# Kernel tuning notes

Measured on AMD Instinct MI355X. Metric: run time of the kernel, lower is better.

Reference implementation:

```python
import jax, jax.numpy as jnp
import numpy as np


def setup_inputs() -> dict:
    key = jax.random.key(0)
    k1, k2 = jax.random.split(key)
    b, n, d = 4, 4096, 512
    m = 4096
    l = max(n, m)
    x = jax.random.normal(k1, (b, n, d), dtype=jnp.float32)
    t = jax.random.normal(k2, (1, 2 * l - 2, d), dtype=jnp.float32)
    return {"x": x, "t": t, "m": m}


def reference(x, t, m):
    # x: (b, n, d); t: (1, 2*max(n,m)-2, d); output: (b, m, d)
    n = x.shape[1]
    l = max(n, m)
    fft_len = 2 * l
    x_fft = jnp.fft.rfft(x, fft_len, axis=-2)   # (b, l+1, d) complex
    t_fft = jnp.fft.rfft(t, fft_len, axis=-2)   # (1, l+1, d) complex
    o = jnp.fft.irfft(x_fft * t_fft, fft_len, axis=-2)[:, :m]
    return o
```

## Files before the change

### kernel.cpp

```cpp
#include <hip/hip_runtime.h>
#include <math.h>

#define N_FFT   8192
#define SEQ     4096
#define NCH     512
#define TLEN    8190

__device__ __forceinline__ float2 cmul(float2 a, float2 b) {
    return make_float2(a.x * b.x - a.y * b.y, a.x * b.y + a.y * b.x);
}
__device__ __forceinline__ float2 cmulj(float2 a, float2 b) {
    return make_float2(a.x * b.x + a.y * b.y, a.y * b.x - a.x * b.y);
}
__device__ __forceinline__ float2 cadd(float2 a, float2 b) {
    return make_float2(a.x + b.x, a.y + b.y);
}
__device__ __forceinline__ float2 csub(float2 a, float2 b) {
    return make_float2(a.x - b.x, a.y - b.y);
}

constexpr float W32C[16] = {
    1.0f, 0.9807852804032304f, 0.9238795325112867f, 0.8314696123025452f,
    0.7071067811865476f, 0.5555702330196023f, 0.3826834323650898f, 0.1950903220161283f,
    0.0f, -0.1950903220161282f, -0.3826834323650897f, -0.5555702330196020f,
    -0.7071067811865475f, -0.8314696123025453f, -0.9238795325112867f, -0.9807852804032304f
};
constexpr float W32S[16] = {
    -0.0f, -0.1950903220161283f, -0.3826834323650898f, -0.5555702330196022f,
    -0.7071067811865476f, -0.8314696123025452f, -0.9238795325112867f, -0.9807852804032304f,
    -1.0f, -0.9807852804032304f, -0.9238795325112867f, -0.8314696123025453f,
    -0.7071067811865476f, -0.5555702330196022f, -0.3826834323650899f, -0.1950903220161286f
};

constexpr int BREV5[32] = {0,16,8,24,4,20,12,28,2,18,10,26,6,22,14,30,
                           1,17,9,25,5,21,13,29,3,19,11,27,7,23,15,31};
constexpr int BREV4[16] = {0,8,4,12,2,10,6,14,1,9,5,13,3,11,7,15};

__device__ __forceinline__ int brev3i(int b) {
    return ((b & 1) << 2) | (b & 2) | ((b & 4) >> 2);
}

__device__ __forceinline__ void fft32_dif(float2 a[32]) {
#pragma unroll
    for (int s = 4; s >= 0; --s) {
        const int h = 1 << s;
#pragma unroll
        for (int g = 0; g < 32; g += 2 * h) {
#pragma unroll
            for (int i = 0; i < h; ++i) {
                float2 x0 = a[g + i], x1 = a[g + i + h];
                a[g + i] = cadd(x0, x1);
                float2 w = make_float2(W32C[i << (4 - s)], W32S[i << (4 - s)]);
                a[g + i + h] = cmul(csub(x0, x1), w);
            }
        }
    }
}

__device__ __forceinline__ void fft16_dif(float2 a[16]) {
#pragma unroll
    for (int s = 3; s >= 0; --s) {
        const int h = 1 << s;
#pragma unroll
        for (int g = 0; g < 16; g += 2 * h) {
#pragma unroll
            for (int i = 0; i < h; ++i) {
                float2 x0 = a[g + i], x1 = a[g + i + h];
                a[g + i] = cadd(x0, x1);
                float2 w = make_float2(W32C[i << (4 - s)], W32S[i << (4 - s)]);
                a[g + i + h] = cmul(csub(x0, x1), w);
            }
        }
    }
}

__device__ __forceinline__ void ifft16_dit(float2 a[16]) {
#pragma unroll
    for (int s = 0; s <= 3; ++s) {
        const int h = 1 << s;
#pragma unroll
        for (int g = 0; g < 16; g += 2 * h) {
#pragma unroll
            for (int i = 0; i < h; ++i) {
                float2 w = make_float2(W32C[i << (4 - s)], -W32S[i << (4 - s)]);
                float2 t = cmul(a[g + i + h], w);
                float2 x0 = a[g + i];
                a[g + i] = cadd(x0, t);
                a[g + i + h] = csub(x0, t);
            }
        }
    }
}

__device__ __forceinline__ void fft8_dif(float2 a[8]) {
#pragma unroll
    for (int s = 2; s >= 0; --s) {
        const int h = 1 << s;
#pragma unroll
        for (int g = 0; g < 8; g += 2 * h) {
#pragma unroll
            for (int i = 0; i < h; ++i) {
                float2 x0 = a[g + i], x1 = a[g + i + h];
                a[g + i] = cadd(x0, x1);
                int e = (i << (2 - s)) << 2;
                float2 w = make_float2(W32C[e], W32S[e]);
                a[g + i + h] = cmul(csub(x0, x1), w);
            }
        }
    }
}

__device__ __forceinline__ int SLOT(int r, int c) {
    return (r << 8) + (c ^ ((c >> 4) & 7) ^ ((r & 1) << 3));
}
__device__ __forceinline__ int ZADDR(int q) {
    return SLOT(q & 31, (((q >> 5) & 31) << 3) + brev3i((q >> 10) & 7));
}
__device__ __forceinline__ int SLOT16(int r, int c) {
    return (r << 8) + (c ^ ((c >> 4) & 7) ^ ((r & 1) << 3));
}

__global__ __launch_bounds__(256) void twiddle_init(float2* __restrict__ tw) {
    int k = blockIdx.x * 256 + threadIdx.x;
    double th = -2.0 * 3.14159265358979323846 * (double)k / (double)N_FFT;
    tw[k] = make_float2((float)cos(th), (float)sin(th));
}

__global__ __launch_bounds__(256) void transpose_in(const float* __restrict__ x,
                                                    const float* __restrict__ t,
                                                    float2* __restrict__ xT,
                                                    float2* __restrict__ tT) {
    __shared__ float tX[64][65], tY[64][65];
    const int tid = threadIdx.x;
    if (blockIdx.x < 1024) {
        const int bid = blockIdx.x;
        const int pb = bid >> 9;
        const int dt = (bid >> 6) & 7;
        const int nt = bid & 63;
        const int d0 = dt << 6, n0 = nt << 6;
        const float* x0 = x + (size_t)(2 * pb) * SEQ * NCH;
        const float* x1 = x0 + (size_t)SEQ * NCH;
        {
            const int c4 = tid & 15, r16 = tid >> 4;
#pragma unroll
            for (int it = 0; it < 4; ++it) {
                int row = r16 + (it << 4);
                size_t off = (size_t)(n0 + row) * NCH + d0 + (c4 << 2);
                float4 v0 = *(const float4*)(x0 + off);
                float4 v1 = *(const float4*)(x1 + off);
                tX[row][(c4 << 2) + 0] = v0.x; tX[row][(c4 << 2) + 1] = v0.y;
                tX[row][(c4 << 2) + 2] = v0.z; tX[row][(c4 << 2) + 3] = v0.w;
                tY[row][(c4 << 2) + 0] = v1.x; tY[row][(c4 << 2) + 1] = v1.y;
                tY[row][(c4 << 2) + 2] = v1.z; tY[row][(c4 << 2) + 3] = v1.w;
            }
        }
        __syncthreads();
        {
            const int nc = tid & 63, dr4 = tid >> 6;
#pragma unroll
            for (int it = 0; it < 16; ++it) {
                int dr = dr4 + (it << 2);
                xT[(((size_t)(pb * NCH + d0 + dr)) << 12) + n0 + nc] =
                    make_float2(tX[nc][dr], tY[nc][dr]);
            }
        }
    } else {
        const int bid = blockIdx.x - 1024;
        const int nt = bid >> 2, dpt = bid & 3;
        const int n0 = nt << 6, dp0 = dpt << 6;
        {
            const int c = tid & 63, r4 = tid >> 6;
#pragma unroll
            for (int it = 0; it < 16; ++it) {
                int row = r4 + (it << 2);
                int nn = n0 + row;
                float2 v = make_float2(0.f, 0.f);
                if (nn < TLEN)
                    v = *(const float2*)(t + (size_t)nn * NCH + ((dp0 + c) << 1));
                tX[row][c] = v.x;
                tY[row][c] = v.y;
            }
        }
        __syncthreads();
        {
            const int nc = tid & 63, dr4 = tid >> 6;
#pragma unroll
            for (int it = 0; it < 16; ++it) {
                int dr = dr4 + (it << 2);
                tT[(((size_t)(dp0 + dr)) << 13) + n0 + nc] =
                    make_float2(tX[nc][dr], tY[nc][dr]);
            }
        }
    }
}

__global__ __launch_bounds__(256) void tfft3_kernel(const float2* __restrict__ tT,
                                                    const float2* __restrict__ tw,
                                                    float2* __restrict__ Tc) {
    __shared__ float2 z[N_FFT];
    const int tid = threadIdx.x;
    const int d0 = blockIdx.x * 2;
    const int d1 = d0 + 1;
    const float2* tp = tT + ((size_t)blockIdx.x << 13);

    float2 a[32];
#pragma unroll
    for (int n1 = 0; n1 < 32; ++n1)
        a[n1] = tp[(n1 << 8) + tid];
    fft32_dif(a);
    {
        float2 w = tw[tid], w2 = cmul(w, w);
        float2 we = make_float2(1.f, 0.f), wo = w;
#pragma unroll
        for (int k1 = 0; k1 < 32; k1 += 2) {
            z[SLOT(k1, tid)]     = (k1 == 0) ? a[0] : cmul(a[BREV5[k1]], we);
            z[SLOT(k1 + 1, tid)] = cmul(a[BREV5[k1 + 1]], wo);
            we = cmul(we, w2); wo = cmul(wo, w2);
        }
    }
    __syncthreads();

    {
        const int r = tid >> 3, n2p = tid & 7;
#pragma unroll
        for (int n1p = 0; n1p < 32; ++n1p)
            a[n1p] = z[SLOT(r, (n1p << 3) + n2p)];
        fft32_dif(a);
        float2 wb = tw[n2p << 5], wb2 = cmul(wb, wb);
        float2 be = make_float2(1.f, 0.f), bo = wb;
#pragma unroll
        for (int k1p = 0; k1p < 32; k1p += 2) {
            z[SLOT(r, (k1p << 3) + n2p)]       = (k1p == 0) ? a[0] : cmul(a[BREV5[k1p]], be);
            z[SLOT(r, ((k1p + 1) << 3) + n2p)] = cmul(a[BREV5[k1p + 1]], bo);
            be = cmul(be, wb2); bo = cmul(bo, wb2);
        }
    }
    __syncthreads();

#pragma unroll
    for (int u = 0; u < 4; ++u) {
        int f = tid + (u << 8);
        int k1 = f >> 5, k1p = f & 31;
        float2 b[8];
#pragma unroll
        for (int e = 0; e < 8; ++e) b[e] = z[SLOT(k1, (k1p << 3) + e)];
        fft8_dif(b);
#pragma unroll
        for (int j = 0; j < 8; ++j) z[SLOT(k1, (k1p << 3) + j)] = b[j];
    }
    __syncthreads();

    const float sc = 0.5f / (float)N_FFT;
#pragma unroll
    for (int v = 0; v < 16; ++v) {
        int p = tid + (v << 8);
        int q   = p >> 9;
        int rem = p & 511;
        int t_  = rem >> 1, e = rem & 1;
        int j_  = (q << 1) + e;
        int kp  = (t_ >> 4) + ((t_ & 15) << 4) + (BREV4[j_] << 8);
#pragma unroll
        for (int par = 0; par < 2; ++par) {
            int k  = 2 * kp + par;
            int km = (N_FFT - k) & (N_FFT - 1);
            float2 A = z[ZADDR(k)];
            float2 B = z[ZADDR(km)];
            float2 Bj = make_float2(B.x, -B.y);
            float2 T0 = make_float2((A.x + Bj.x) * sc, (A.y + Bj.y) * sc);
            float2 dd = csub(A, Bj);
            float2 T1 = make_float2(dd.y * sc, -dd.x * sc);
            Tc[(size_t)d0 * N_FFT + (par << 12) + p] = T0;
            Tc[(size_t)d1 * N_FFT + (par << 12) + p] = T1;
        }
    }
}

__global__ __launch_bounds__(512, 2) void conv5_kernel(float2* __restrict__ xoT,
                                                       const float2* __restrict__ tw,
                                                       const float2* __restrict__ Tc) {
    __shared__ float2 z[2 * SEQ];
    const int tid = threadIdx.x;
    const int par = tid >> 8;
    const int t   = tid & 255;
    const int d   = blockIdx.x;
    float2* zb = z + (par << 12);

    float2 a[16];

#pragma unroll
    for (int pb = 0; pb < 2; ++pb) {
        if (pb == 1) __syncthreads();
        const float2* xp = xoT + ((size_t)(pb * NCH + d) << 12);

        if (par == 0) {
#pragma unroll
            for (int n1 = 0; n1 < 16; ++n1)
                a[n1] = xp[(n1 << 8) + t];
        } else {
#pragma unroll
            for (int n1 = 0; n1 < 16; ++n1)
                a[n1] = cmul(xp[(n1 << 8) + t], tw[(n1 << 8) + t]);
        }
        fft16_dif(a);
        {
            float2 w = tw[2 * t];
            float2 w2 = cmul(w, w);
            float2 we = make_float2(1.f, 0.f), wo = w;
#pragma unroll
            for (int k1 = 0; k1 < 16; k1 += 2) {
                zb[SLOT16(k1, t)]     = (k1 == 0) ? a[0] : cmul(a[BREV4[k1]], we);
                zb[SLOT16(k1 + 1, t)] = cmul(a[BREV4[k1 + 1]], wo);
                we = cmul(we, w2); wo = cmul(wo, w2);
            }
        }
        __syncthreads();

        {
            const int k1 = t >> 4, n3 = t & 15;
#pragma unroll
            for (int n2 = 0; n2 < 16; ++n2)
                a[n2] = zb[SLOT16(k1, (n2 << 4) + n3)];
            fft16_dif(a);
            float2 wb = tw[n3 << 5];
            float2 wb2 = cmul(wb, wb);
            float2 be = make_float2(1.f, 0.f), bo = wb;
#pragma unroll
            for (int r1 = 0; r1 < 16; r1 += 2) {
                zb[SLOT16(k1, (r1 << 4) + n3)]       = (r1 == 0) ? a[0] : cmul(a[BREV4[r1]], be);
                zb[SLOT16(k1, ((r1 + 1) << 4) + n3)] = cmul(a[BREV4[r1 + 1]], bo);
                be = cmul(be, wb2); bo = cmul(bo, wb2);
            }
        }
        __builtin_amdgcn_sched_barrier(0);

        {
            const int k1 = t >> 4, r1 = t & 15;
#pragma unroll
            for (int n3 = 0; n3 < 16; ++n3)
                a[n3] = zb[SLOT16(k1, (r1 << 4) + n3)];
            fft16_dif(a);
            const float4* tp = (const float4*)(Tc + ((size_t)d << 13) + (par << 12));
#pragma unroll
            for (int q = 0; q < 8; ++q) {
                float4 f4 = tp[(q << 8) + t];
                a[2 * q]     = cmul(a[2 * q],     make_float2(f4.x, f4.y));
                a[2 * q + 1] = cmul(a[2 * q + 1], make_float2(f4.z, f4.w));
            }
            ifft16_dit(a);
#pragma unroll
            for (int n3 = 0; n3 < 16; ++n3)
                zb[SLOT16(k1, (r1 << 4) + n3)] = a[n3];
        }
        __builtin_amdgcn_sched_barrier(0);

        {
            const int k1 = t >> 4, n3 = t & 15;
            float2 wb = tw[n3 << 5], wb2 = cmul(wb, wb);
            float2 be = make_float2(1.f, 0.f), bo = wb;
#pragma unroll
            for (int r1 = 0; r1 < 16; r1 += 2) {
                float2 v0 = zb[SLOT16(k1, (r1 << 4) + n3)];
                float2 v1 = zb[SLOT16(k1, ((r1 + 1) << 4) + n3)];
                a[BREV4[r1]]     = (r1 == 0) ? v0 : cmulj(v0, be);
                a[BREV4[r1 + 1]] = cmulj(v1, bo);
                be = cmul(be, wb2); bo = cmul(bo, wb2);
            }
            ifft16_dit(a);
#pragma unroll
            for (int n2 = 0; n2 < 16; ++n2)
                zb[SLOT16(k1, (n2 << 4) + n3)] = a[n2];
        }
        __syncthreads();

        {
            float2 w = tw[2 * t], w2 = cmul(w, w);
            float2 we = make_float2(1.f, 0.f), wo = w;
#pragma unroll
            for (int k1 = 0; k1 < 16; k1 += 2) {
                float2 v0 = zb[SLOT16(k1, t)];
                float2 v1 = zb[SLOT16(k1 + 1, t)];
                a[BREV4[k1]]     = (k1 == 0) ? v0 : cmulj(v0, we);
                a[BREV4[k1 + 1]] = cmulj(v1, wo);
                we = cmul(we, w2); wo = cmul(wo, w2);
            }
            ifft16_dit(a);
        }
        __syncthreads();

        if (par == 0) {
#pragma unroll
            for (int n1 = 8; n1 < 16; ++n1)
                zb[((n1 - 8) << 8) + t] = a[n1];
        } else {
#pragma unroll
            for (int n1 = 0; n1 < 8; ++n1)
                zb[(n1 << 8) + t] = a[n1];
        }
        __syncthreads();

        {
            float2* xw = xoT + ((size_t)(pb * NCH + d) << 12);
            if (par == 0) {
#pragma unroll
                for (int n1 = 0; n1 < 8; ++n1) {
                    int n = (n1 << 8) + t;
                    float2 uo = z[SEQ + (n1 << 8) + t];
                    xw[n] = cadd(a[n1], cmulj(uo, tw[n]));
                }
            } else {
#pragma unroll
                for (int n1 = 8; n1 < 16; ++n1) {
                    int n = (n1 << 8) + t;
                    float2 ue = z[((n1 - 8) << 8) + t];
                    xw[n] = cadd(ue, cmulj(a[n1], tw[n]));
                }
            }
        }
    }
}

__global__ __launch_bounds__(256) void transpose_out(const float2* __restrict__ oT,
                                                     float* __restrict__ out) {
    __shared__ float2 tile[32][65];
    const int tid = threadIdx.x;
    const int bid = blockIdx.x;
    const int pb = bid >> 10;
    const int dt = (bid >> 6) & 15;
    const int nt = bid & 63;
    const int d0 = dt << 5, n0 = nt << 6;

    {
        const int nl = tid & 63, dl = tid >> 6;
#pragma unroll
        for (int i = 0; i < 8; ++i) {
            int dd = dl + (i << 2);
            tile[dd][nl] = oT[(((size_t)(pb * NCH + d0 + dd)) << 12) + n0 + nl];
        }
    }
    __syncthreads();
    {
        const int dl = tid & 31, ns = tid >> 5;
        float* o0 = out + (size_t)(2 * pb) * SEQ * NCH;
        float* o1 = o0 + (size_t)SEQ * NCH;
#pragma unroll
        for (int j = 0; j < 8; ++j) {
            int nn = n0 + ns + (j << 3);
            float2 v = tile[dl][ns + (j << 3)];
            o0[(size_t)nn * NCH + d0 + dl] = v.x;
            o1[(size_t)nn * NCH + d0 + dl] = v.y;
        }
    }
}

__global__ __launch_bounds__(256) void tfft2_kernel(const float* __restrict__ t,
                                                    const float2* __restrict__ tw,
                                                    float2* __restrict__ Tc) {
    __shared__ float2 z[N_FFT];
    const int tid = threadIdx.x;
    const int d0 = blockIdx.x * 2;
    const int d1 = d0 + 1;

    float2 a[32];
#pragma unroll
    for (int n1 = 0; n1 < 32; ++n1) {
        int n = (n1 << 8) + tid;
        float va = 0.f, vb = 0.f;
        if (n < TLEN) {
            va = t[(size_t)n * NCH + d0];
            vb = t[(size_t)n * NCH + d1];
        }
        a[n1] = make_float2(va, vb);
    }
    fft32_dif(a);
    {
        float2 w = tw[tid], w2 = cmul(w, w);
        float2 we = make_float2(1.f, 0.f), wo = w;
#pragma unroll
        for (int k1 = 0; k1 < 32; k1 += 2) {
            z[SLOT(k1, tid)]     = (k1 == 0) ? a[0] : cmul(a[BREV5[k1]], we);
            z[SLOT(k1 + 1, tid)] = cmul(a[BREV5[k1 + 1]], wo);
            we = cmul(we, w2); wo = cmul(wo, w2);
        }
    }
    __syncthreads();
    {
        const int r = tid >> 3, n2p = tid & 7;
#pragma unroll
        for (int n1p = 0; n1p < 32; ++n1p)
            a[n1p] = z[SLOT(r, (n1p << 3) + n2p)];
        fft32_dif(a);
        float2 wb = tw[n2p << 5], wb2 = cmul(wb, wb);
        float2 be = make_float2(1.f, 0.f), bo = wb;
#pragma unroll
        for (int k1p = 0; k1p < 32; k1p += 2) {
            z[SLOT(r, (k1p << 3) + n2p)]       = (k1p == 0) ? a[0] : cmul(a[BREV5[k1p]], be);
            z[SLOT(r, ((k1p + 1) << 3) + n2p)] = cmul(a[BREV5[k1p + 1]], bo);
            be = cmul(be, wb2); bo = cmul(bo, wb2);
        }
    }
    __syncthreads();
#pragma unroll
    for (int u = 0; u < 4; ++u) {
        int f = tid + (u << 8);
        int k1 = f >> 5, k1p = f & 31;
        float2 b[8];
#pragma unroll
        for (int e = 0; e < 8; ++e) b[e] = z[SLOT(k1, (k1p << 3) + e)];
        fft8_dif(b);
#pragma unroll
        for (int j = 0; j < 8; ++j) z[SLOT(k1, (k1p << 3) + j)] = b[j];
    }
    __syncthreads();

    const float sc = 0.5f / (float)N_FFT;
#pragma unroll
    for (int v = 0; v < 16; ++v) {
        int s = tid + (v << 8);
        int k1 = s >> 8, r1 = (s >> 4) & 15, j = s & 15;
        int kp = k1 + (r1 << 4) + (BREV4[j] << 8);
#pragma unroll
        for (int par = 0; par < 2; ++par) {
            int k  = 2 * kp + par;
            int km = (N_FFT - k) & (N_FFT - 1);
            float2 A = z[ZADDR(k)];
            float2 B = z[ZADDR(km)];
            float2 Bj = make_float2(B.x, -B.y);
            float2 T0 = make_float2((A.x + Bj.x) * sc, (A.y + Bj.y) * sc);
            float2 dd = csub(A, Bj);
            float2 T1 = make_float2(dd.y * sc, -dd.x * sc);
            Tc[(size_t)d0 * N_FFT + (par << 12) + s] = T0;
            Tc[(size_t)d1 * N_FFT + (par << 12) + s] = T1;
        }
    }
}

template<bool OT>
__global__ __launch_bounds__(256, 2) void conv3_kernel(const float* __restrict__ x,
                                                       const float2* __restrict__ tw,
                                                       const float2* __restrict__ Tc,
                                                       float2* __restrict__ oT,
                                                       float* __restrict__ out) {
    __shared__ float2 z[SEQ];
    const int tid = threadIdx.x;
    const int sb = (blockIdx.x & 7) * 128 + (blockIdx.x >> 3);
    const int d  = sb >> 1;
    const int pb = sb & 1;

    const float* x0 = x + (size_t)(2 * pb) * SEQ * NCH + d;
    const float* x1 = x0 + (size_t)SEQ * NCH;

    float2 a[16], ie[16];

#pragma unroll
    for (int par = 0; par < 2; ++par) {
        if (par == 1) __syncthreads();

        if (par == 0) {
#pragma unroll
            for (int n1 = 0; n1 < 16; ++n1) {
                int n = (n1 << 8) + tid;
                a[n1] = make_float2(x0[(size_t)n * NCH], x1[(size_t)n * NCH]);
            }
        } else {
#pragma unroll
            for (int n1 = 0; n1 < 16; ++n1) {
                int n = (n1 << 8) + tid;
                float2 v = make_float2(x0[(size_t)n * NCH], x1[(size_t)n * NCH]);
                a[n1] = cmul(v, tw[n]);
            }
        }
        fft16_dif(a);
        {
            float2 w = tw[2 * tid], w2 = cmul(w, w);
            float2 we = make_float2(1.f, 0.f), wo = w;
#pragma unroll
            for (int k1 = 0; k1 < 16; k1 += 2) {
                z[SLOT16(k1, tid)]     = (k1 == 0) ? a[0] : cmul(a[BREV4[k1]], we);
                z[SLOT16(k1 + 1, tid)] = cmul(a[BREV4[k1 + 1]], wo);
                we = cmul(we, w2); wo = cmul(wo, w2);
            }
        }
        __syncthreads();
        {
            const int k1 = tid >> 4, n3 = tid & 15;
#pragma unroll
            for (int n2 = 0; n2 < 16; ++n2)
                a[n2] = z[SLOT16(k1, (n2 << 4) + n3)];
            fft16_dif(a);
            float2 wb = tw[n3 << 5], wb2 = cmul(wb, wb);
            float2 be = make_float2(1.f, 0.f), bo = wb;
#pragma unroll
            for (int r1 = 0; r1 < 16; r1 += 2) {
                z[SLOT16(k1, (r1 << 4) + n3)]       = (r1 == 0) ? a[0] : cmul(a[BREV4[r1]], be);
                z[SLOT16(k1, ((r1 + 1) << 4) + n3)] = cmul(a[BREV4[r1 + 1]], bo);
                be = cmul(be, wb2); bo = cmul(bo, wb2);
            }
        }
        __syncthreads();
        {
            const int k1 = tid >> 4, r1 = tid & 15;
#pragma unroll
            for (int n3 = 0; n3 < 16; ++n3)
                a[n3] = z[SLOT16(k1, (r1 << 4) + n3)];
            fft16_dif(a);
            const float2* Td = Tc + ((size_t)d << 13) + (par << 12);
#pragma unroll
            for (int j = 0; j < 16; ++j) {
                float2 T = Td[(tid << 4) + j];
                a[j] = cmul(a[j], T);
            }
            ifft16_dit(a);
#pragma unroll
            for (int n3 = 0; n3 < 16; ++n3)
                z[SLOT16(k1, (r1 << 4) + n3)] = a[n3];
        }
        __syncthreads();
        {
            const int k1 = tid >> 4, n3 = tid & 15;
            float2 wb = tw[n3 << 5], wb2 = cmul(wb, wb);
            float2 be = make_float2(1.f, 0.f), bo = wb;
#pragma unroll
            for (int r1 = 0; r1 < 16; r1 += 2) {
                float2 v0 = z[SLOT16(k1, (r1 << 4) + n3)];
                float2 v1 = z[SLOT16(k1, ((r1 + 1) << 4) + n3)];
                a[BREV4[r1]]     = (r1 == 0) ? v0 : cmulj(v0, be);
                a[BREV4[r1 + 1]] = cmulj(v1, bo);
                be = cmul(be, wb2); bo = cmul(bo, wb2);
            }
            ifft16_dit(a);
#pragma unroll
            for (int n2 = 0; n2 < 16; ++n2)
                z[SLOT16(k1, (n2 << 4) + n3)] = a[n2];
        }
        __syncthreads();
        {
            float2 w = tw[2 * tid], w2 = cmul(w, w);
            float2 we = make_float2(1.f, 0.f), wo = w;
#pragma unroll
            for (int k1 = 0; k1 < 16; k1 += 2) {
                float2 v0 = z[SLOT16(k1, tid)];
                float2 v1 = z[SLOT16(k1 + 1, tid)];
                a[BREV4[k1]]     = (k1 == 0) ? v0 : cmulj(v0, we);
                a[BREV4[k1 + 1]] = cmulj(v1, wo);
                we = cmul(we, w2); wo = cmul(wo, w2);
            }
            ifft16_dit(a);
        }

        if (par == 0) {
#pragma unroll
            for (int n1 = 0; n1 < 16; ++n1) ie[n1] = a[n1];
        } else {
            if constexpr (OT) {
                float2* op = oT + (((size_t)(pb * NCH + d)) << 12);
#pragma unroll
                for (int n1 = 0; n1 < 16; ++n1) {
                    int n = (n1 << 8) + tid;
                    op[n] = cadd(ie[n1], cmulj(a[n1], tw[n]));
                }
            } else {
                float* o0 = out + (size_t)(2 * pb) * SEQ * NCH + d;
                float* o1 = o0 + (size_t)SEQ * NCH;
#pragma unroll
                for (int n1 = 0; n1 < 16; ++n1) {
                    int n = (n1 << 8) + tid;
                    float2 o = cadd(ie[n1], cmulj(a[n1], tw[n]));
                    o0[(size_t)n * NCH] = o.x;
                    o1[(size_t)n * NCH] = o.y;
                }
            }
        }
    }
}

extern "C" void kernel_launch(void* const* d_in, const int* in_sizes, int n_in,
                              void* d_out, int out_size, void* d_ws, size_t ws_size,
                              hipStream_t stream) {
    (void)in_sizes; (void)n_in; (void)out_size;
    const float* x = (const float*)d_in[0];
    const float* t = (const float*)d_in[1];
    float* out = (float*)d_out;

    float2* tw  = (float2*)d_ws;
    float2* Tc  = tw + N_FFT;
    float2* xoT = Tc + (size_t)NCH * N_FFT;
    float2* tT  = xoT + 2ull * NCH * SEQ;

    const size_t need_full = sizeof(float2) * ((size_t)N_FFT + (size_t)NCH * N_FFT
                                               + 2ull * NCH * SEQ
                                               + 256ull * N_FFT);
    const size_t need_ot   = sizeof(float2) * ((size_t)N_FFT + (size_t)NCH * N_FFT
                                               + 2ull * NCH * SEQ);

    twiddle_init<<<N_FFT / 256, 256, 0, stream>>>(tw);
    if (ws_size >= need_full) {
        transpose_in<<<1536, 256, 0, stream>>>(x, t, xoT, tT);
        tfft3_kernel<<<NCH / 2, 256, 0, stream>>>(tT, tw, Tc);
        conv5_kernel<<<NCH, 512, 0, stream>>>(xoT, tw, Tc);
        transpose_out<<<2048, 256, 0, stream>>>(xoT, out);
    } else if (ws_size >= need_ot) {
        tfft2_kernel<<<NCH / 2, 256, 0, stream>>>(t, tw, Tc);
        conv3_kernel<true><<<1024, 256, 0, stream>>>(x, tw, Tc, xoT, out);
        transpose_out<<<2048, 256, 0, stream>>>(xoT, out);
    } else {
        tfft2_kernel<<<NCH / 2, 256, 0, stream>>>(t, tw, Tc);
        conv3_kernel<false><<<1024, 256, 0, stream>>>(x, tw, Tc, nullptr, out);
    }
}
```

Measured before the change: 102.3 us.

## Split conv kernel into 256-thread blocks per channel-batch with sequential parities

```diff
diff --git a/kernel.cpp b/kernel.cpp
--- a/kernel.cpp
+++ b/kernel.cpp
@@ -275,23 +275,22 @@
     }
 }
 
-__global__ __launch_bounds__(512, 2) void conv5_kernel(float2* __restrict__ xoT,
+__global__ __launch_bounds__(256, 4) void conv6_kernel(float2* __restrict__ xoT,
                                                        const float2* __restrict__ tw,
-                                                       const float2* __restrict__ Tc) {
-    __shared__ float2 z[2 * SEQ];
-    const int tid = threadIdx.x;
-    const int par = tid >> 8;
-    const int t   = tid & 255;
-    const int d   = blockIdx.x;
-    float2* zb = z + (par << 12);
-
-    float2 a[16];
-
-#pragma unroll
-    for (int pb = 0; pb < 2; ++pb) {
-        if (pb == 1) __syncthreads();
-        const float2* xp = xoT + ((size_t)(pb * NCH + d) << 12);
-
+                                                       const float2* __restrict__ Tc,
+                                                       float2* __restrict__ scrbuf) {
+    __shared__ float2 z[SEQ];
+    const int t = threadIdx.x;
+    const int sb = (blockIdx.x & 7) * 128 + (blockIdx.x >> 3);
+    const int d  = sb >> 1;
+    const int pb = sb & 1;
+    float2* xp  = xoT + ((size_t)(pb * NCH + d) << 12);
+    float2* scr = scrbuf + ((size_t)sb << 11);
+
+    float2 a[16], ie[8];
+
+#pragma unroll
+    for (int par = 0; par < 2; ++par) {
         if (par == 0) {
 #pragma unroll
             for (int n1 = 0; n1 < 16; ++n1)
@@ -308,8 +307,8 @@
             float2 we = make_float2(1.f, 0.f), wo = w;
 #pragma unroll
             for (int k1 = 0; k1 < 16; k1 += 2) {
-                zb[SLOT16(k1, t)]     = (k1 == 0) ? a[0] : cmul(a[BREV4[k1]], we);
-                zb[SLOT16(k1 + 1, t)] = cmul(a[BREV4[k1 + 1]], wo);
+                z[SLOT16(k1, t)]     = (k1 == 0) ? a[0] : cmul(a[BREV4[k1]], we);
+                z[SLOT16(k1 + 1, t)] = cmul(a[BREV4[k1 + 1]], wo);
                 we = cmul(we, w2); wo = cmul(wo, w2);
             }
         }
@@ -319,15 +318,15 @@
             const int k1 = t >> 4, n3 = t & 15;
 #pragma unroll
             for (int n2 = 0; n2 < 16; ++n2)
-                a[n2] = zb[SLOT16(k1, (n2 << 4) + n3)];
+                a[n2] = z[SLOT16(k1, (n2 << 4) + n3)];
             fft16_dif(a);
             float2 wb = tw[n3 << 5];
             float2 wb2 = cmul(wb, wb);
             float2 be = make_float2(1.f, 0.f), bo = wb;
 #pragma unroll
             for (int r1 = 0; r1 < 16; r1 += 2) {
-                zb[SLOT16(k1, (r1 << 4) + n3)]       = (r1 == 0) ? a[0] : cmul(a[BREV4[r1]], be);
-                zb[SLOT16(k1, ((r1 + 1) << 4) + n3)] = cmul(a[BREV4[r1 + 1]], bo);
+                z[SLOT16(k1, (r1 << 4) + n3)]       = (r1 == 0) ? a[0] : cmul(a[BREV4[r1]], be);
+                z[SLOT16(k1, ((r1 + 1) << 4) + n3)] = cmul(a[BREV4[r1 + 1]], bo);
                 be = cmul(be, wb2); bo = cmul(bo, wb2);
             }
         }
@@ -337,7 +336,7 @@
             const int k1 = t >> 4, r1 = t & 15;
 #pragma unroll
             for (int n3 = 0; n3 < 16; ++n3)
-                a[n3] = zb[SLOT16(k1, (r1 << 4) + n3)];
+                a[n3] = z[SLOT16(k1, (r1 << 4) + n3)];
             fft16_dif(a);
             const float4* tp = (const float4*)(Tc + ((size_t)d << 13) + (par << 12));
 #pragma unroll
@@ -349,7 +348,7 @@
             ifft16_dit(a);
 #pragma unroll
             for (int n3 = 0; n3 < 16; ++n3)
-                zb[SLOT16(k1, (r1 << 4) + n3)] = a[n3];
+                z[SLOT16(k1, (r1 << 4) + n3)] = a[n3];
         }
         __builtin_amdgcn_sched_barrier(0);
 
@@ -359,8 +358,8 @@
             float2 be = make_float2(1.f, 0.f), bo = wb;
 #pragma unroll
             for (int r1 = 0; r1 < 16; r1 += 2) {
-                float2 v0 = zb[SLOT16(k1, (r1 << 4) + n3)];
-                float2 v1 = zb[SLOT16(k1, ((r1 + 1) << 4) + n3)];
+                float2 v0 = z[SLOT16(k1, (r1 << 4) + n3)];
+                float2 v1 = z[SLOT16(k1, ((r1 + 1) << 4) + n3)];
                 a[BREV4[r1]]     = (r1 == 0) ? v0 : cmulj(v0, be);
                 a[BREV4[r1 + 1]] = cmulj(v1, bo);
                 be = cmul(be, wb2); bo = cmul(bo, wb2);
@@ -368,7 +367,7 @@
             ifft16_dit(a);
 #pragma unroll
             for (int n2 = 0; n2 < 16; ++n2)
-                zb[SLOT16(k1, (n2 << 4) + n3)] = a[n2];
+                z[SLOT16(k1, (n2 << 4) + n3)] = a[n2];
         }
         __syncthreads();
 
@@ -377,43 +376,32 @@
             float2 we = make_float2(1.f, 0.f), wo = w;
 #pragma unroll
             for (int k1 = 0; k1 < 16; k1 += 2) {
-                float2 v0 = zb[SLOT16(k1, t)];
-                float2 v1 = zb[SLOT16(k1 + 1, t)];
+                float2 v0 = z[SLOT16(k1, t)];
+                float2 v1 = z[SLOT16(k1 + 1, t)];
                 a[BREV4[k1]]     = (k1 == 0) ? v0 : cmulj(v0, we);
                 a[BREV4[k1 + 1]] = cmulj(v1, wo);
                 we = cmul(we, w2); wo = cmul(wo, w2);
             }
             ifft16_dit(a);
         }
-        __syncthreads();
 
         if (par == 0) {
 #pragma unroll
+            for (int n1 = 0; n1 < 8; ++n1) ie[n1] = a[n1];
+#pragma unroll
             for (int n1 = 8; n1 < 16; ++n1)
-                zb[((n1 - 8) << 8) + t] = a[n1];
+                scr[((n1 - 8) << 8) + t] = a[n1];
         } else {
 #pragma unroll
-            for (int n1 = 0; n1 < 8; ++n1)
-                zb[(n1 << 8) + t] = a[n1];
-        }
-        __syncthreads();
-
-        {
-            float2* xw = xoT + ((size_t)(pb * NCH + d) << 12);
-            if (par == 0) {
-#pragma unroll
-                for (int n1 = 0; n1 < 8; ++n1) {
-                    int n = (n1 << 8) + t;
-                    float2 uo = z[SEQ + (n1 << 8) + t];
-                    xw[n] = cadd(a[n1], cmulj(uo, tw[n]));
-                }
-            } else {
-#pragma unroll
-                for (int n1 = 8; n1 < 16; ++n1) {
-                    int n = (n1 << 8) + t;
-                    float2 ue = z[((n1 - 8) << 8) + t];
-                    xw[n] = cadd(ue, cmulj(a[n1], tw[n]));
-                }
+            for (int n1 = 0; n1 < 8; ++n1) {
+                int n = (n1 << 8) + t;
+                xp[n] = cadd(ie[n1], cmulj(a[n1], tw[n]));
+            }
+#pragma unroll
+            for (int n1 = 8; n1 < 16; ++n1) {
+                int n = (n1 << 8) + t;
+                float2 ue = scr[((n1 - 8) << 8) + t];
+                xp[n] = cadd(ue, cmulj(a[n1], tw[n]));
             }
         }
     }
@@ -606,7 +594,7 @@
             const float2* Td = Tc + ((size_t)d << 13) + (par << 12);
 #pragma unroll
             for (int j = 0; j < 16; ++j) {
-                float2 T = Td[(tid << 4) + j];
+                float2 T = Td[((tid >> 4) << 8) + ((tid & 15) << 4) + j];
                 a[j] = cmul(a[j], T);
             }
             ifft16_dit(a);
@@ -696,7 +684,7 @@
     if (ws_size >= need_full) {
         transpose_in<<<1536, 256, 0, stream>>>(x, t, xoT, tT);
         tfft3_kernel<<<NCH / 2, 256, 0, stream>>>(tT, tw, Tc);
-        conv5_kernel<<<NCH, 512, 0, stream>>>(xoT, tw, Tc);
+        conv6_kernel<<<1024, 256, 0, stream>>>(xoT, tw, Tc, tT);
         transpose_out<<<2048, 256, 0, stream>>>(xoT, out);
     } else if (ws_size >= need_ot) {
         tfft2_kernel<<<NCH / 2, 256, 0, stream>>>(t, tw, Tc);
```

New measurement: 113.7 us. 11.1% more time.
